# Kernel tuning notes

Hardware: AMD Instinct MI355X
Metric: run time of the kernel (lower is better)

## Reference

```python
import jax, jax.numpy as jnp
import numpy as np

EPS_GEN = 1e-7   # GENConv message epsilon
LN_EPS = 1e-5    # torch LayerNorm default eps


def _ln(x, g, b):
    mu = x.mean(-1, keepdims=True)
    v = ((x - mu) ** 2).mean(-1, keepdims=True)
    return (x - mu) / jnp.sqrt(v + LN_EPS) * g + b


def _genconv(x, src, dst, N, t, W1, b1, g1, be1, W2, b2):
    # GENConv(aggr='softmax', learn_t, num_layers=2, norm='layer'), no edge_attr
    msg = jax.nn.relu(x[src]) + EPS_GEN                 # [E,H] gather + eps
    z = msg * t
    m = jax.ops.segment_max(z, dst, num_segments=N)      # scatter-max [N,H]
    e = jnp.exp(z - m[dst])
    denom = jax.ops.segment_sum(e, dst, num_segments=N) + 1e-16
    alpha = e / denom[dst]                               # per-neighborhood softmax
    out = jax.ops.segment_sum(msg * alpha, dst, num_segments=N) + x  # aggregate + root
    h = jax.nn.relu(_ln(out @ W1 + b1, g1, be1))         # MLP [H,2H] + LN + ReLU
    return h @ W2 + b2                                   # [2H,H] plain last layer


def setup_inputs():
    key = jax.random.key(0)
    ks = jax.random.split(key, 24)
    N, E, Fin, H = 100000, 1600000, 16, 64
    s = 0.02
    d = {
        'x': jax.random.normal(ks[0], (N, Fin), jnp.float32),
        'edge_index': jax.random.randint(ks[1], (2, E), 0, N, dtype=jnp.int32),
        'W_enc': jax.random.normal(ks[2], (Fin, H), jnp.float32) * s,
        'b_enc': jnp.zeros((H,), jnp.float32),
        't1': jnp.float32(1.0),
        'W1a': jax.random.normal(ks[3], (H, 2 * H), jnp.float32) * s,
        'b1a': jnp.zeros((2 * H,), jnp.float32),
        'g1a': jnp.ones((2 * H,), jnp.float32),
        'be1a': jnp.zeros((2 * H,), jnp.float32),
        'W1b': jax.random.normal(ks[4], (2 * H, H), jnp.float32) * s,
        'b1b': jnp.zeros((H,), jnp.float32),
        'g_n1': jnp.ones((H,), jnp.float32),
        'b_n1': jnp.zeros((H,), jnp.float32),
        't2': jnp.float32(1.0),
        'W2a': jax.random.normal(ks[5], (H, 2 * H), jnp.float32) * s,
        'b2a': jnp.zeros((2 * H,), jnp.float32),
        'g2a': jnp.ones((2 * H,), jnp.float32),
        'be2a': jnp.zeros((2 * H,), jnp.float32),
        'W2b': jax.random.normal(ks[6], (2 * H, H), jnp.float32) * s,
        'b2b': jnp.zeros((H,), jnp.float32),
        'g_n0': jnp.ones((H,), jnp.float32),
        'b_n0': jnp.zeros((H,), jnp.float32),
        'W_lin': jax.random.normal(ks[7], (H, 1), jnp.float32) * s,
        'b_lin': jnp.zeros((1,), jnp.float32),
    }
    return d


def reference(x, edge_index, W_enc, b_enc, t1, W1a, b1a, g1a, be1a, W1b, b1b,
              g_n1, b_n1, t2, W2a, b2a, g2a, be2a, W2b, b2b, g_n0, b_n0,
              W_lin, b_lin):
    N = x.shape[0]
    src, dst = edge_index[0], edge_index[1]
    h = x @ W_enc + b_enc                                   # node encoder
    h = _genconv(h, src, dst, N, t1, W1a, b1a, g1a, be1a, W1b, b1b)  # layers[0].conv (bare)
    # layers[1]: DeepGCNLayer res+ -> x + conv(act(norm(x)))  (dropout = identity, deterministic ref)
    r = _genconv(jax.nn.relu(_ln(h, g_n1, b_n1)), src, dst, N, t2,
                 W2a, b2a, g2a, be2a, W2b, b2b)
    h = h + r
    h = jax.nn.relu(_ln(h, g_n0, b_n0))                     # layers[0].norm / act at the end
    logits = h @ W_lin + b_lin                              # [N,1]
    return jax.nn.sigmoid(logits), logits
```

## Files before the change

kernel.cpp:

```cpp
#include <hip/hip_runtime.h>
#include <hip/hip_fp16.h>
#include <math.h>

constexpr int HD   = 64;
constexpr int HD2  = 128;
constexpr int SCAP = 48;
constexpr int NPW  = 4;
constexpr int NPB  = 16;
constexpr int PSH  = 14;
constexpr int EPB  = 2048;

constexpr int SO = 68;
constexpr int SU = 132;
constexpr int SY = 68;

constexpr float FXS  = 8192.f;
constexpr float FXSI = 1.f / 8192.f;
constexpr float RXS  = 16384.f;
constexpr float RXSI = 1.f / 16384.f;
constexpr float HXS  = 4096.f;
constexpr float HXSI = 1.f / 4096.f;

typedef short  bf16x8 __attribute__((ext_vector_type(8)));
typedef float  f32x4  __attribute__((ext_vector_type(4)));

__device__ __forceinline__ float wave_sum(float v) {
#pragma unroll
    for (int off = 32; off > 0; off >>= 1) v += __shfl_xor(v, off, 64);
    return v;
}

__device__ __forceinline__ unsigned int packme(float v, float t) {
    int q = (int)(fmaxf(v, 0.f) * FXS + 0.5f);
    unsigned int mu = (unsigned int)min(q, 65535);
    float m = fmaf((float)mu, FXSI, 1e-7f);
    float e = __expf(m * t);
    __half eh = __float2half(e);
    unsigned short eu = *(unsigned short*)&eh;
    return (mu << 16) | (unsigned int)eu;
}

__device__ __forceinline__ float h2f_lo(unsigned int w) {
    unsigned short lo = (unsigned short)(w & 0xffffu);
    __half h = *(__half*)&lo;
    return __half2float(h);
}

__device__ __forceinline__ short f2s16(float v, float s) {
    int q = (int)rintf(v * s);
    return (short)max(-32768, min(32767, q));
}

__device__ __forceinline__ void splitf(float f, short& hi, short& lo) {
    unsigned u = __float_as_uint(f);
    hi = (short)(u >> 16);
    float lf = f - __uint_as_float(u & 0xffff0000u);
    lo = (short)(__float_as_uint(lf) >> 16);
}

__device__ __forceinline__ void split8(const float* p, bf16x8& hi, bf16x8& lo) {
    float v[8];
    *(float4*)&v[0] = *(const float4*)p;
    *(float4*)&v[4] = *(const float4*)(p + 4);
#pragma unroll
    for (int j = 0; j < 8; j++) { short h, l; splitf(v[j], h, l); hi[j] = h; lo[j] = l; }
}

__global__ void prep_kernel(const int* __restrict__ ei,
                            int* __restrict__ cursor, int* __restrict__ slots,
                            const float* __restrict__ x,
                            const float* __restrict__ W,
                            const float* __restrict__ b,
                            const float* __restrict__ t1ptr,
                            short* __restrict__ h0s,
                            unsigned int* __restrict__ g,
                            const float* __restrict__ L1W1, const float* __restrict__ L1W2,
                            const float* __restrict__ L2W1, const float* __restrict__ L2W2,
                            short* __restrict__ swz,
                            int E, int N, int SB, int encB) {
    if (blockIdx.x < (unsigned)SB) {
        int p = blockIdx.x & 7;
        int base = (blockIdx.x >> 3) * EPB;
        for (int off = threadIdx.x; off < EPB; off += 256) {
            int e = base + off;
            if (e < E) {
                int dst = ei[E + e];
                if ((dst >> PSH) == p) {
                    int src = ei[e];
                    int pos = atomicAdd(&cursor[dst], 1);
                    if (pos < SCAP) slots[(unsigned)(dst * SCAP + pos)] = src;
                }
            }
        }
    } else if (blockIdx.x < (unsigned)(SB + encB)) {
        int i = (blockIdx.x - SB) * 256 + threadIdx.x;
        if (i >= N * HD) return;
        int n = i >> 6, j = i & 63;
        float t1v = t1ptr[0];
        const float* xr = x + (unsigned)(n * 16);
        float acc = b[j];
#pragma unroll
        for (int k = 0; k < 16; k++) acc += xr[k] * W[k * HD + j];
        h0s[i] = f2s16(acc, RXS);
        g[i] = packme(acc, t1v);
    } else {
        int sb = blockIdx.x - SB - encB;
        int layer = sb >> 3;
        int idx = (sb & 7) * 256 + threadIdx.x;
        const float* Wa = layer ? L2W1 : L1W1;
        const float* Wb = layer ? L2W2 : L1W2;
        short* base = swz + layer * 32768;
        if (idx < 1024) {
            int ks = idx >> 9, rem = idx & 511;
            int nt = rem >> 6, lane = rem & 63;
#pragma unroll
            for (int j = 0; j < 8; j++) {
                int k = ks * 32 + (lane >> 4) * 8 + j;
                int n = nt * 16 + (lane & 15);
                short hh, ll; splitf(Wa[k * HD2 + n], hh, ll);
                base[idx * 8 + j] = hh; base[8192 + idx * 8 + j] = ll;
            }
        } else {
            int jdx = idx - 1024;
            int ks = jdx >> 8, rem = jdx & 255;
            int nt = rem >> 6, lane = rem & 63;
#pragma unroll
            for (int j = 0; j < 8; j++) {
                int k = ks * 32 + (lane >> 4) * 8 + j;
                int n = nt * 16 + (lane & 15);
                short hh, ll; splitf(Wb[k * HD + n], hh, ll);
                base[16384 + jdx * 8 + j] = hh; base[24576 + jdx * 8 + j] = ll;
            }
        }
    }
}

template <int MODE>
__global__ void __launch_bounds__(256) conv_kernel(
    const unsigned int* __restrict__ gin,
    const short* __restrict__ hroot,
    const int* __restrict__ deg_arr, const int* __restrict__ slots,
    const float* __restrict__ tnext,
    const short* __restrict__ W1hi, const short* __restrict__ W1lo,
    const float* __restrict__ b1,
    const float* __restrict__ g1, const float* __restrict__ be1,
    const short* __restrict__ W2hi, const short* __restrict__ W2lo,
    const float* __restrict__ b2,
    const float* __restrict__ gn, const float* __restrict__ bn,
    const short* __restrict__ resid,
    const float* __restrict__ wlin, const float* __restrict__ blin,
    float* __restrict__ outA, short* __restrict__ outH,
    unsigned int* __restrict__ outG, int N) {
    __shared__ float s_out[NPB][SO];
    __shared__ float s_u[NPB][SU];
    __shared__ float s_y[NPB][SY];
    int wv = threadIdx.x >> 6, j = threadIdx.x & 63;
    int q = j >> 4;
    int c = (j & 15) << 2;
    int nb = blockIdx.x * NPB + wv * NPW;
    float tn = (MODE == 0) ? tnext[0] : 0.f;

    int deg[NPW], sid[NPW];
#pragma unroll
    for (int u = 0; u < NPW; u++) {
        int n = nb + u;
        int d = (n < N) ? min(deg_arr[n], SCAP) : 0;
        deg[u] = d;
        sid[u] = (j < d) ? slots[(unsigned)(n * SCAP + j)] : 0;
    }
#pragma unroll
    for (int u = 0; u < NPW; u++) {
        int n = nb + u;
        int bl = wv * NPW + u;
        if (n < N) {
            int d = deg[u];
            float4 ae = {0.f, 0.f, 0.f, 0.f}, aw = {0.f, 0.f, 0.f, 0.f};
            for (int base = 0; base < d; base += 16) {
                uint4 uv[4];
#pragma unroll
                for (int bb = 0; bb < 4; bb++) {
                    int i = base + bb * 4 + q;
                    int s = __shfl(sid[u], i, 64);
                    uv[bb] = *(const uint4*)(gin + (unsigned)((s << 6) | c));
                }
#pragma unroll
                for (int bb = 0; bb < 4; bb++) {
                    int i = base + bb * 4 + q;
                    if (i < d) {
                        uint4 w = uv[bb];
                        float m0 = (float)(w.x >> 16), e0 = h2f_lo(w.x);
                        float m1 = (float)(w.y >> 16), e1 = h2f_lo(w.y);
                        float m2 = (float)(w.z >> 16), e2 = h2f_lo(w.z);
                        float m3 = (float)(w.w >> 16), e3 = h2f_lo(w.w);
                        ae.x += e0; ae.y += e1; ae.z += e2; ae.w += e3;
                        aw.x = fmaf(m0, e0, aw.x); aw.y = fmaf(m1, e1, aw.y);
                        aw.z = fmaf(m2, e2, aw.z); aw.w = fmaf(m3, e3, aw.w);
                    }
                }
            }
#pragma unroll
            for (int off = 16; off <= 32; off <<= 1) {
                ae.x += __shfl_xor(ae.x, off, 64); ae.y += __shfl_xor(ae.y, off, 64);
                ae.z += __shfl_xor(ae.z, off, 64); ae.w += __shfl_xor(ae.w, off, 64);
                aw.x += __shfl_xor(aw.x, off, 64); aw.y += __shfl_xor(aw.y, off, 64);
                aw.z += __shfl_xor(aw.z, off, 64); aw.w += __shfl_xor(aw.w, off, 64);
            }
            if (q == 0) {
                float4 o;
                float n0 = fmaf(ae.x, 1e-7f, aw.x * FXSI);
                float n1 = fmaf(ae.y, 1e-7f, aw.y * FXSI);
                float n2 = fmaf(ae.z, 1e-7f, aw.z * FXSI);
                float n3 = fmaf(ae.w, 1e-7f, aw.w * FXSI);
                if (MODE == 0) {
                    short4 hv = *(const short4*)(hroot + (unsigned)((n << 6) | c));
                    o.x = n0 / (ae.x + 1e-16f) + (float)hv.x * RXSI;
                    o.y = n1 / (ae.y + 1e-16f) + (float)hv.y * RXSI;
                    o.z = n2 / (ae.z + 1e-16f) + (float)hv.z * RXSI;
                    o.w = n3 / (ae.w + 1e-16f) + (float)hv.w * RXSI;
                } else {
                    uint4 w = *(const uint4*)(gin + (unsigned)((n << 6) | c));
                    o.x = n0 / (ae.x + 1e-16f) + (float)(w.x >> 16) * FXSI;
                    o.y = n1 / (ae.y + 1e-16f) + (float)(w.y >> 16) * FXSI;
                    o.z = n2 / (ae.z + 1e-16f) + (float)(w.z >> 16) * FXSI;
                    o.w = n3 / (ae.w + 1e-16f) + (float)(w.w >> 16) * FXSI;
                }
                *(float4*)&s_out[bl][c] = o;
            }
        } else if (q == 0) {
            float4 z = {0.f, 0.f, 0.f, 0.f};
            *(float4*)&s_out[bl][c] = z;
        }
    }
    __syncthreads();

    int mrow = j & 15, kq = j >> 4, ncol = j & 15;
    {
        f32x4 acc[2];
#pragma unroll
        for (int i = 0; i < 2; i++) {
            float bb = b1[(wv * 2 + i) * 16 + ncol];
            acc[i] = (f32x4){bb, bb, bb, bb};
        }
#pragma unroll
        for (int ks = 0; ks < 2; ks++) {
            bf16x8 ah, al;
            split8(&s_out[mrow][ks * 32 + kq * 8], ah, al);
#pragma unroll
            for (int i = 0; i < 2; i++) {
                int nt = wv * 2 + i;
                int fo = (((ks * 8 + nt) * 64 + j) << 3);
                bf16x8 bh = *(const bf16x8*)(W1hi + fo);
                bf16x8 bl = *(const bf16x8*)(W1lo + fo);
                acc[i] = __builtin_amdgcn_mfma_f32_16x16x32_bf16(al, bh, acc[i], 0, 0, 0);
                acc[i] = __builtin_amdgcn_mfma_f32_16x16x32_bf16(ah, bl, acc[i], 0, 0, 0);
                acc[i] = __builtin_amdgcn_mfma_f32_16x16x32_bf16(ah, bh, acc[i], 0, 0, 0);
            }
        }
#pragma unroll
        for (int i = 0; i < 2; i++)
#pragma unroll
            for (int r = 0; r < 4; r++)
                s_u[kq * 4 + r][(wv * 2 + i) * 16 + ncol] = acc[i][r];
    }
    __syncthreads();

    {
        float g1a_ = g1[j], g1b_ = g1[HD + j];
        float be1a_ = be1[j], be1b_ = be1[HD + j];
#pragma unroll
        for (int u = 0; u < NPW; u++) {
            int bl = wv * NPW + u;
            float u0 = s_u[bl][j], u1 = s_u[bl][HD + j];
            float mu = wave_sum(u0 + u1) * (1.f / HD2);
            float d0 = u0 - mu, d1 = u1 - mu;
            float var = wave_sum(d0 * d0 + d1 * d1) * (1.f / HD2);
            float rstd = rsqrtf(var + 1e-5f);
            s_u[bl][j]      = fmaxf(d0 * rstd * g1a_ + be1a_, 0.f);
            s_u[bl][HD + j] = fmaxf(d1 * rstd * g1b_ + be1b_, 0.f);
        }
    }
    __syncthreads();

    {
        float bb = b2[wv * 16 + ncol];
        f32x4 acc = (f32x4){bb, bb, bb, bb};
#pragma unroll
        for (int ks = 0; ks < 4; ks++) {
            bf16x8 ah, al;
            split8(&s_u[mrow][ks * 32 + kq * 8], ah, al);
            int fo = (((ks * 4 + wv) * 64 + j) << 3);
            bf16x8 bh = *(const bf16x8*)(W2hi + fo);
            bf16x8 bl = *(const bf16x8*)(W2lo + fo);
            acc = __builtin_amdgcn_mfma_f32_16x16x32_bf16(al, bh, acc, 0, 0, 0);
            acc = __builtin_amdgcn_mfma_f32_16x16x32_bf16(ah, bl, acc, 0, 0, 0);
            acc = __builtin_amdgcn_mfma_f32_16x16x32_bf16(ah, bh, acc, 0, 0, 0);
        }
#pragma unroll
        for (int r = 0; r < 4; r++)
            s_y[kq * 4 + r][wv * 16 + ncol] = acc[r];
    }
    __syncthreads();

    float gn_ = gn[j], bn_ = bn[j];
    float wl = (MODE == 1) ? wlin[j] : 0.f;
#pragma unroll
    for (int u = 0; u < NPW; u++) {
        int n = nb + u;
        if (n >= N) continue;
        float yv = s_y[wv * NPW + u][j];
        unsigned oidx = (unsigned)((n << 6) | j);
        if (MODE == 0) {
            outH[oidx] = f2s16(yv, HXS);
            float mu = wave_sum(yv) * (1.f / HD);
            float d = yv - mu;
            float var = wave_sum(d * d) * (1.f / HD);
            float rstd = rsqrtf(var + 1e-5f);
            outG[oidx] = packme(d * rstd * gn_ + bn_, tn);
        } else {
            float hf = yv + (float)resid[oidx] * HXSI;
            float mu = wave_sum(hf) * (1.f / HD);
            float d = hf - mu;
            float var = wave_sum(d * d) * (1.f / HD);
            float rstd = rsqrtf(var + 1e-5f);
            float h2 = fmaxf(d * rstd * gn_ + bn_, 0.f);
            float dot = wave_sum(h2 * wl);
            if (j == 0) {
                float logit = dot + blin[0];
                outA[n] = 1.f / (1.f + __expf(-logit));
                outA[N + n] = logit;
            }
        }
    }
}

extern "C" void kernel_launch(void* const* d_in, const int* in_sizes, int n_in,
                              void* d_out, int out_size, void* d_ws, size_t ws_size,
                              hipStream_t stream) {
    const float* x     = (const float*)d_in[0];
    const int*   ei    = (const int*)  d_in[1];
    const float* W_enc = (const float*)d_in[2];
    const float* b_enc = (const float*)d_in[3];
    const float* t1    = (const float*)d_in[4];
    const float* W1a   = (const float*)d_in[5];
    const float* b1a   = (const float*)d_in[6];
    const float* g1a   = (const float*)d_in[7];
    const float* be1a  = (const float*)d_in[8];
    const float* W1b   = (const float*)d_in[9];
    const float* b1b   = (const float*)d_in[10];
    const float* g_n1  = (const float*)d_in[11];
    const float* b_n1  = (const float*)d_in[12];
    const float* t2    = (const float*)d_in[13];
    const float* W2a   = (const float*)d_in[14];
    const float* b2a   = (const float*)d_in[15];
    const float* g2a   = (const float*)d_in[16];
    const float* be2a  = (const float*)d_in[17];
    const float* W2b   = (const float*)d_in[18];
    const float* b2b   = (const float*)d_in[19];
    const float* g_n0  = (const float*)d_in[20];
    const float* b_n0  = (const float*)d_in[21];
    const float* W_lin = (const float*)d_in[22];
    const float* b_lin = (const float*)d_in[23];

    int N = in_sizes[0] / 16;
    int E = in_sizes[1] / 2;
    size_t NH = (size_t)N * HD;

    short* h0s          = (short*)d_ws;
    short* h1s          = h0s + NH;
    unsigned int* g0    = (unsigned int*)(h1s + NH);
    unsigned int* g1f   = g0 + NH;
    int*   cursor       = (int*)(g1f + NH);
    int*   slots        = cursor + N;
    short* swz          = (short*)(slots + (size_t)N * SCAP);

    int nodeBlocks = (N + NPB - 1) / NPB;
    int chunks     = (E + EPB - 1) / EPB;
    int SB         = chunks * 8;
    int encBlocks  = (int)((NH + 255) / 256);

    hipMemsetAsync(cursor, 0, (size_t)N * sizeof(int), stream);

    prep_kernel<<<SB + encBlocks + 16, 256, 0, stream>>>(
        ei, cursor, slots, x, W_enc, b_enc, t1, h0s, g0,
        W1a, W1b, W2a, W2b, swz, E, N, SB, encBlocks);

    short* W1hi_1 = swz,          *W1lo_1 = swz + 8192;
    short* W2hi_1 = swz + 16384,  *W2lo_1 = swz + 24576;
    short* W1hi_2 = swz + 32768,  *W1lo_2 = swz + 40960;
    short* W2hi_2 = swz + 49152,  *W2lo_2 = swz + 57344;

    conv_kernel<0><<<nodeBlocks, 256, 0, stream>>>(
        g0, h0s, cursor, slots, t2,
        W1hi_1, W1lo_1, b1a, g1a, be1a, W2hi_1, W2lo_1, b1b,
        g_n1, b_n1, nullptr, nullptr, nullptr,
        nullptr, h1s, g1f, N);

    conv_kernel<1><<<nodeBlocks, 256, 0, stream>>>(
        g1f, nullptr, cursor, slots, t2,
        W1hi_2, W1lo_2, b2a, g2a, be2a, W2hi_2, W2lo_2, b2b,
        g_n0, b_n0, h1s, W_lin, b_lin,
        (float*)d_out, nullptr, nullptr, N);
}
```

Measured before the change: 388.0 us.

## Store only quantized messages and recompute exp in gather loop

```diff
diff --git a/kernel.cpp b/kernel.cpp
--- a/kernel.cpp
+++ b/kernel.cpp
@@ -21,6 +21,14 @@
 constexpr float HXS  = 4096.f;
 constexpr float HXSI = 1.f / 4096.f;
 
+#if __has_builtin(__builtin_amdgcn_exp2f)
+#define FEXP2(x) __builtin_amdgcn_exp2f(x)
+#define EXP_SCALE 1.4426950408889634f
+#else
+#define FEXP2(x) __expf(x)
+#define EXP_SCALE 1.0f
+#endif
+
 typedef short  bf16x8 __attribute__((ext_vector_type(8)));
 typedef float  f32x4  __attribute__((ext_vector_type(4)));
 
@@ -30,20 +38,9 @@
     return v;
 }
 
-__device__ __forceinline__ unsigned int packme(float v, float t) {
+__device__ __forceinline__ unsigned short packm(float v) {
     int q = (int)(fmaxf(v, 0.f) * FXS + 0.5f);
-    unsigned int mu = (unsigned int)min(q, 65535);
-    float m = fmaf((float)mu, FXSI, 1e-7f);
-    float e = __expf(m * t);
-    __half eh = __float2half(e);
-    unsigned short eu = *(unsigned short*)&eh;
-    return (mu << 16) | (unsigned int)eu;
-}
-
-__device__ __forceinline__ float h2f_lo(unsigned int w) {
-    unsigned short lo = (unsigned short)(w & 0xffffu);
-    __half h = *(__half*)&lo;
-    return __half2float(h);
+    return (unsigned short)min(q, 65535);
 }
 
 __device__ __forceinline__ short f2s16(float v, float s) {
@@ -71,38 +68,43 @@
                             const float* __restrict__ x,
                             const float* __restrict__ W,
                             const float* __restrict__ b,
-                            const float* __restrict__ t1ptr,
                             short* __restrict__ h0s,
-                            unsigned int* __restrict__ g,
+                            unsigned short* __restrict__ g,
                             const float* __restrict__ L1W1, const float* __restrict__ L1W2,
                             const float* __restrict__ L2W1, const float* __restrict__ L2W2,
                             short* __restrict__ swz,
                             int E, int N, int SB, int encB) {
     if (blockIdx.x < (unsigned)SB) {
-        int p = blockIdx.x & 7;
-        int base = (blockIdx.x >> 3) * EPB;
-        for (int off = threadIdx.x; off < EPB; off += 256) {
-            int e = base + off;
-            if (e < E) {
-                int dst = ei[E + e];
-                if ((dst >> PSH) == p) {
-                    int src = ei[e];
-                    int pos = atomicAdd(&cursor[dst], 1);
-                    if (pos < SCAP) slots[(unsigned)(dst * SCAP + pos)] = src;
-                }
+        int chunks = SB >> 3;
+        int p  = blockIdx.x / chunks;
+        int ck = blockIdx.x - p * chunks;
+        int e0 = ck * EPB + threadIdx.x;
+        int d8[8], s8[8];
+#pragma unroll
+        for (int it = 0; it < 8; it++) {
+            int e = e0 + it * 256;
+            bool v = (e < E);
+            d8[it] = v ? ei[E + e] : -1;
+            s8[it] = v ? ei[e] : 0;
+        }
+#pragma unroll
+        for (int it = 0; it < 8; it++) {
+            int dst = d8[it];
+            if (dst >= 0 && (dst >> PSH) == p) {
+                int pos = atomicAdd(&cursor[dst], 1);
+                if (pos < SCAP) slots[(unsigned)(dst * SCAP + pos)] = s8[it];
             }
         }
     } else if (blockIdx.x < (unsigned)(SB + encB)) {
         int i = (blockIdx.x - SB) * 256 + threadIdx.x;
         if (i >= N * HD) return;
         int n = i >> 6, j = i & 63;
-        float t1v = t1ptr[0];
         const float* xr = x + (unsigned)(n * 16);
         float acc = b[j];
 #pragma unroll
         for (int k = 0; k < 16; k++) acc += xr[k] * W[k * HD + j];
         h0s[i] = f2s16(acc, RXS);
-        g[i] = packme(acc, t1v);
+        g[i] = packm(acc);
     } else {
         int sb = blockIdx.x - SB - encB;
         int layer = sb >> 3;
@@ -137,10 +139,10 @@
 
 template <int MODE>
 __global__ void __launch_bounds__(256) conv_kernel(
-    const unsigned int* __restrict__ gin,
+    const unsigned short* __restrict__ gin,
     const short* __restrict__ hroot,
     const int* __restrict__ deg_arr, const int* __restrict__ slots,
-    const float* __restrict__ tnext,
+    const float* __restrict__ tcur,
     const short* __restrict__ W1hi, const short* __restrict__ W1lo,
     const float* __restrict__ b1,
     const float* __restrict__ g1, const float* __restrict__ be1,
@@ -150,7 +152,7 @@
     const short* __restrict__ resid,
     const float* __restrict__ wlin, const float* __restrict__ blin,
     float* __restrict__ outA, short* __restrict__ outH,
-    unsigned int* __restrict__ outG, int N) {
+    unsigned short* __restrict__ outG, int N) {
     __shared__ float s_out[NPB][SO];
     __shared__ float s_u[NPB][SU];
     __shared__ float s_y[NPB][SY];
@@ -158,7 +160,7 @@
     int q = j >> 4;
     int c = (j & 15) << 2;
     int nb = blockIdx.x * NPB + wv * NPW;
-    float tn = (MODE == 0) ? tnext[0] : 0.f;
+    float cexp = tcur[0] * (FXSI * EXP_SCALE);
 
     int deg[NPW], sid[NPW];
 #pragma unroll
@@ -176,22 +178,24 @@
             int d = deg[u];
             float4 ae = {0.f, 0.f, 0.f, 0.f}, aw = {0.f, 0.f, 0.f, 0.f};
             for (int base = 0; base < d; base += 16) {
-                uint4 uv[4];
+                uint2 uv[4];
 #pragma unroll
                 for (int bb = 0; bb < 4; bb++) {
                     int i = base + bb * 4 + q;
                     int s = __shfl(sid[u], i, 64);
-                    uv[bb] = *(const uint4*)(gin + (unsigned)((s << 6) | c));
+                    uv[bb] = *(const uint2*)(gin + (unsigned)((s << 6) | c));
                 }
 #pragma unroll
                 for (int bb = 0; bb < 4; bb++) {
                     int i = base + bb * 4 + q;
                     if (i < d) {
-                        uint4 w = uv[bb];
-                        float m0 = (float)(w.x >> 16), e0 = h2f_lo(w.x);
-                        float m1 = (float)(w.y >> 16), e1 = h2f_lo(w.y);
-                        float m2 = (float)(w.z >> 16), e2 = h2f_lo(w.z);
-                        float m3 = (float)(w.w >> 16), e3 = h2f_lo(w.w);
+                        uint2 w = uv[bb];
+                        float m0 = (float)(w.x & 0xffffu), m1 = (float)(w.x >> 16);
+                        float m2 = (float)(w.y & 0xffffu), m3 = (float)(w.y >> 16);
+                        float e0 = FEXP2(m0 * cexp);
+                        float e1 = FEXP2(m1 * cexp);
+                        float e2 = FEXP2(m2 * cexp);
+                        float e3 = FEXP2(m3 * cexp);
                         ae.x += e0; ae.y += e1; ae.z += e2; ae.w += e3;
                         aw.x = fmaf(m0, e0, aw.x); aw.y = fmaf(m1, e1, aw.y);
                         aw.z = fmaf(m2, e2, aw.z); aw.w = fmaf(m3, e3, aw.w);
@@ -218,11 +222,11 @@
                     o.z = n2 / (ae.z + 1e-16f) + (float)hv.z * RXSI;
                     o.w = n3 / (ae.w + 1e-16f) + (float)hv.w * RXSI;
                 } else {
-                    uint4 w = *(const uint4*)(gin + (unsigned)((n << 6) | c));
-                    o.x = n0 / (ae.x + 1e-16f) + (float)(w.x >> 16) * FXSI;
-                    o.y = n1 / (ae.y + 1e-16f) + (float)(w.y >> 16) * FXSI;
-                    o.z = n2 / (ae.z + 1e-16f) + (float)(w.z >> 16) * FXSI;
-                    o.w = n3 / (ae.w + 1e-16f) + (float)(w.w >> 16) * FXSI;
+                    ushort4 rv = *(const ushort4*)(gin + (unsigned)((n << 6) | c));
+                    o.x = n0 / (ae.x + 1e-16f) + (float)rv.x * FXSI;
+                    o.y = n1 / (ae.y + 1e-16f) + (float)rv.y * FXSI;
+                    o.z = n2 / (ae.z + 1e-16f) + (float)rv.z * FXSI;
+                    o.w = n3 / (ae.w + 1e-16f) + (float)rv.w * FXSI;
                 }
                 *(float4*)&s_out[bl][c] = o;
             }
@@ -315,7 +319,7 @@
             float d = yv - mu;
             float var = wave_sum(d * d) * (1.f / HD);
             float rstd = rsqrtf(var + 1e-5f);
-            outG[oidx] = packme(d * rstd * gn_ + bn_, tn);
+            outG[oidx] = packm(d * rstd * gn_ + bn_);
         } else {
             float hf = yv + (float)resid[oidx] * HXSI;
             float mu = wave_sum(hf) * (1.f / HD);
@@ -367,8 +371,8 @@
 
     short* h0s          = (short*)d_ws;
     short* h1s          = h0s + NH;
-    unsigned int* g0    = (unsigned int*)(h1s + NH);
-    unsigned int* g1f   = g0 + NH;
+    unsigned short* g0  = (unsigned short*)(h1s + NH);
+    unsigned short* g1f = g0 + NH;
     int*   cursor       = (int*)(g1f + NH);
     int*   slots        = cursor + N;
     short* swz          = (short*)(slots + (size_t)N * SCAP);
@@ -381,7 +385,7 @@
     hipMemsetAsync(cursor, 0, (size_t)N * sizeof(int), stream);
 
     prep_kernel<<<SB + encBlocks + 16, 256, 0, stream>>>(
-        ei, cursor, slots, x, W_enc, b_enc, t1, h0s, g0,
+        ei, cursor, slots, x, W_enc, b_enc, h0s, g0,
         W1a, W1b, W2a, W2b, swz, E, N, SB, encBlocks);
 
     short* W1hi_1 = swz,          *W1lo_1 = swz + 8192;
@@ -390,7 +394,7 @@
     short* W2hi_2 = swz + 49152,  *W2lo_2 = swz + 57344;
 
     conv_kernel<0><<<nodeBlocks, 256, 0, stream>>>(
-        g0, h0s, cursor, slots, t2,
+        g0, h0s, cursor, slots, t1,
         W1hi_1, W1lo_1, b1a, g1a, be1a, W2hi_1, W2lo_1, b1b,
         g_n1, b_n1, nullptr, nullptr, nullptr,
         nullptr, h1s, g1f, N);
```

Measured after the change: 396.9 us. +2.3%, slower.
